# Kernel optimization log

Measured on AMD Instinct MI355X. Metric: run time of the kernel, lower is better.

## Reference

```python
import jax, jax.numpy as jnp
import numpy as np

B, S, D = 4, 1024, 2048
H, KVH, HD = 32, 8, 64
N_REP = H // KVH  # 4
ROPE_THETA = 1000000.0


def _rope_tables(seq_len, head_dim, theta):
    inv_freq = 1.0 / (theta ** (np.arange(0, head_dim, 2, dtype=np.float32) / head_dim))
    t = np.arange(seq_len, dtype=np.float32)
    freqs = np.outer(t, inv_freq)                      # (S, HD/2)
    emb = np.concatenate([freqs, freqs], axis=-1)      # (S, HD)
    return jnp.asarray(np.cos(emb)), jnp.asarray(np.sin(emb))


def setup_inputs() -> dict:
    key = jax.random.key(0)
    kx, kq, kk, kv, ko = jax.random.split(key, 5)
    cos, sin = _rope_tables(S, HD, ROPE_THETA)
    s = 0.02
    return {
        "x": jax.random.normal(kx, (B, S, D), jnp.float32),
        "cos": cos,
        "sin": sin,
        "Wq": jax.random.normal(kq, (D, H * HD), jnp.float32) * s,
        "Wk": jax.random.normal(kk, (D, KVH * HD), jnp.float32) * s,
        "Wv": jax.random.normal(kv, (D, KVH * HD), jnp.float32) * s,
        "Wo": jax.random.normal(ko, (H * HD, D), jnp.float32) * s,
    }


def _rotate_half(t):
    t1, t2 = jnp.split(t, 2, axis=-1)
    return jnp.concatenate([-t2, t1], axis=-1)


def reference(x, cos, sin, Wq, Wk, Wv, Wo):
    # projections
    q = (x @ Wq).reshape(B, S, H, HD)      # (b, s, h, d)
    k = (x @ Wk).reshape(B, S, KVH, HD)
    v = (x @ Wv).reshape(B, S, KVH, HD)

    # RoPE: cos/sin (s, d) broadcast over heads (unsqueeze_dim=1 -> (s,1,d))
    c = cos[:, None, :]
    sn = sin[:, None, :]
    q = q * c + _rotate_half(q) * sn
    k = k * c + _rotate_half(k) * sn

    # GQA attention without physically repeating KV:
    # q grouped as (b, kvh, n_rep, s, d); repeat_kv '(h r)' maps q head g*n_rep+r -> kv head g
    qg = q.transpose(0, 2, 1, 3).reshape(B, KVH, N_REP, S, HD)
    kt = k.transpose(0, 2, 1, 3)  # (b, kvh, s, d)
    vt = v.transpose(0, 2, 1, 3)

    scale = 1.0 / jnp.sqrt(jnp.asarray(HD, x.dtype))
    scores = jnp.einsum('bgrqd,bgkd->bgrqk', qg, kt) * scale  # (b, kvh, rep, s, s)
    probs = jax.nn.softmax(scores, axis=-1)
    out = jnp.einsum('bgrqk,bgkd->bgrqd', probs, vt)           # (b, kvh, rep, s, d)

    out = out.reshape(B, H, S, HD).transpose(0, 2, 1, 3).reshape(B, S, H * HD)
    return out @ Wo
```

## Files before the change

### kernel.cpp

```cpp
#include <hip/hip_runtime.h>

typedef unsigned short u16;
typedef __attribute__((ext_vector_type(8))) __bf16 bf16x8;
typedef __attribute__((ext_vector_type(4))) _Float16 f16x4;
typedef __attribute__((ext_vector_type(8))) _Float16 f16x8;
typedef __attribute__((ext_vector_type(4))) float f32x4;

#define BB 4
#define SS 1024
#define DD 2048
#define HH 32
#define KVHN 8
#define HDIM 64

__device__ __forceinline__ u16 f2b(float f) {
    union { float f; unsigned u; } v; v.f = f;
    unsigned r = v.u + 0x7FFFu + ((v.u >> 16) & 1u);
    return (u16)(r >> 16);
}
__device__ __forceinline__ float b2f(u16 h) {
    union { unsigned u; float f; } v; v.u = ((unsigned)h) << 16; return v.f;
}

__device__ __forceinline__ f32x4 mfma16(bf16x8 a, bf16x8 b, f32x4 c) {
    return __builtin_amdgcn_mfma_f32_16x16x32_bf16(a, b, c, 0, 0, 0);
}
__device__ __forceinline__ f32x4 mfma16h(f16x8 a, f16x8 b, f32x4 c) {
    return __builtin_amdgcn_mfma_f32_16x16x32_f16(a, b, c, 0, 0, 0);
}

__device__ __forceinline__ void async_cp16(const void* g, void* l) {
    __builtin_amdgcn_global_load_lds((__attribute__((address_space(1))) void*)g,
                                     (__attribute__((address_space(3))) void*)l,
                                     16, 0, 0);
}

__device__ __forceinline__ f16x8 pack8_f16(const float* p) {
    union { unsigned u[4]; f16x8 v; } pu;
    pu.u[0] = __builtin_bit_cast(unsigned, __builtin_amdgcn_cvt_pkrtz(p[0], p[1]));
    pu.u[1] = __builtin_bit_cast(unsigned, __builtin_amdgcn_cvt_pkrtz(p[2], p[3]));
    pu.u[2] = __builtin_bit_cast(unsigned, __builtin_amdgcn_cvt_pkrtz(p[4], p[5]));
    pu.u[3] = __builtin_bit_cast(unsigned, __builtin_amdgcn_cvt_pkrtz(p[6], p[7]));
    return pu.v;
}

__global__ __launch_bounds__(256) void cast_x_kernel(const float* __restrict__ x,
                                                     u16* __restrict__ xb) {
    int i = (blockIdx.x * 256 + threadIdx.x) * 4;
    float4 v = *(const float4*)(x + i);
    unsigned r0 = (unsigned)f2b(v.x) | ((unsigned)f2b(v.y) << 16);
    unsigned r1 = (unsigned)f2b(v.z) | ((unsigned)f2b(v.w) << 16);
    *(uint2*)(xb + i) = make_uint2(r0, r1);
}

__global__ __launch_bounds__(256) void wtrans_all_kernel(const float* __restrict__ Wq,
                                                         const float* __restrict__ Wk,
                                                         const float* __restrict__ Wv,
                                                         const float* __restrict__ Wo,
                                                         u16* __restrict__ Wqkvt,
                                                         u16* __restrict__ Wot) {
    __shared__ float tile[32][33];
    int z = blockIdx.z;
    const float* W = (z == 0) ? Wq : (z == 1) ? Wk : (z == 2) ? Wv : Wo;
    int N = (z == 1 || z == 2) ? 512 : 2048;
    int n_off = (z == 1) ? 2048 : (z == 2) ? 2560 : 0;
    u16* Wt = (z == 3) ? Wot : Wqkvt;
    int n0 = blockIdx.x * 32;
    if (n0 >= N) return;
    int k0 = blockIdx.y * 32;
    int tid = threadIdx.x;
    int nj = tid & 31;
    int ki = tid >> 5;
#pragma unroll
    for (int it = 0; it < 4; it++) {
        int kk = it * 8 + ki;
        tile[kk][nj] = W[(size_t)(k0 + kk) * N + n0 + nj];
    }
    __syncthreads();
#pragma unroll
    for (int it = 0; it < 4; it++) {
        int nn = it * 8 + ki;
        Wt[(size_t)(n0 + nn + n_off) * 2048 + k0 + nj] = f2b(tile[nj][nn]);
    }
}

template <int OUT_BF16>
__device__ __forceinline__ void gemm_bt_body(const u16* __restrict__ A,
                                             const u16* __restrict__ Bt,
                                             void* __restrict__ Cv,
                                             int M, int N, int K) {
    __shared__ __align__(16) u16 As[128 * 64];
    __shared__ __align__(16) u16 Bs[128 * 64];
    const int tid = threadIdx.x;
    const int lane = tid & 63;
    const int w = tid >> 6;
    const int m0 = blockIdx.y * 128;
    const int n0 = blockIdx.x * 128;
    const int wm = (w >> 1) * 64;
    const int wn = (w & 1) * 64;
    const int lr = lane & 15;
    const int lg = lane >> 4;
    const int lq = lg * 4;

    const f32x4 zero4 = {0.f, 0.f, 0.f, 0.f};
    f32x4 acc[4][4];
#pragma unroll
    for (int i = 0; i < 4; i++)
#pragma unroll
        for (int j = 0; j < 4; j++) acc[i][j] = zero4;

    for (int k0 = 0; k0 < K; k0 += 64) {
#pragma unroll
        for (int sh = 0; sh < 4; sh++) {
            int i_lin = sh * 256 + tid;
            int row = i_lin >> 3;
            int c = i_lin & 7;
            int cs = c ^ (row & 7);
            async_cp16(A + (size_t)(m0 + row) * K + k0 + cs * 8, As + sh * 2048 + w * 512);
            async_cp16(Bt + (size_t)(n0 + row) * K + k0 + cs * 8, Bs + sh * 2048 + w * 512);
        }
        __syncthreads();
#pragma unroll
        for (int kb = 0; kb < 2; kb++) {
            bf16x8 af[4], bfr[4];
#pragma unroll
            for (int mi = 0; mi < 4; mi++) {
                int r = wm + mi * 16 + lr;
                af[mi] = *(const bf16x8*)(As + r * 64 + (((kb * 4 + lg) ^ (r & 7)) * 8));
            }
#pragma unroll
            for (int ni = 0; ni < 4; ni++) {
                int r = wn + ni * 16 + lr;
                bfr[ni] = *(const bf16x8*)(Bs + r * 64 + (((kb * 4 + lg) ^ (r & 7)) * 8));
            }
#pragma unroll
            for (int mi = 0; mi < 4; mi++)
#pragma unroll
                for (int ni = 0; ni < 4; ni++)
                    acc[mi][ni] = mfma16(af[mi], bfr[ni], acc[mi][ni]);
        }
        __syncthreads();
    }

    if (OUT_BF16) {
        u16* C = (u16*)Cv;
#pragma unroll
        for (int mi = 0; mi < 4; mi++)
#pragma unroll
            for (int ni = 0; ni < 4; ni++)
#pragma unroll
                for (int i = 0; i < 4; i++) {
                    int r = m0 + wm + mi * 16 + lq + i;
                    int c = n0 + wn + ni * 16 + lr;
                    C[(size_t)r * N + c] = f2b(acc[mi][ni][i]);
                }
    } else {
        float* C = (float*)Cv;
#pragma unroll
        for (int mi = 0; mi < 4; mi++)
#pragma unroll
            for (int ni = 0; ni < 4; ni++)
#pragma unroll
                for (int i = 0; i < 4; i++) {
                    int r = m0 + wm + mi * 16 + lq + i;
                    int c = n0 + wn + ni * 16 + lr;
                    C[(size_t)r * N + c] = acc[mi][ni][i];
                }
    }
}

__global__ __launch_bounds__(256) void gemm_qkv(const u16* __restrict__ A,
                                                const u16* __restrict__ Bt,
                                                void* __restrict__ Cv,
                                                int M, int N, int K) {
    gemm_bt_body<1>(A, Bt, Cv, M, N, K);
}

__global__ __launch_bounds__(256) void gemm_out(const u16* __restrict__ A,
                                                const u16* __restrict__ Bt,
                                                void* __restrict__ Cv,
                                                int M, int N, int K) {
    gemm_bt_body<0>(A, Bt, Cv, M, N, K);
}

__global__ __launch_bounds__(256) void rope_kernel(const u16* __restrict__ QKV,
                                                   const float* __restrict__ cosT,
                                                   const float* __restrict__ sinT,
                                                   u16* __restrict__ Qh,
                                                   u16* __restrict__ Kh) {
    const float QSC = 0.125f * 1.44269504088896f;
    int idx = blockIdx.x * 256 + threadIdx.x;
    int d = idx & 31;
    int t = idx >> 5;
    int hh = t % 40;
    int row = t / 40;
    int s = row & (SS - 1);
    int b = row >> 10;
    float c = cosT[s * HDIM + d];
    float sn = sinT[s * HDIM + d];
    if (hh < 32) {
        const u16* src = QKV + (size_t)row * 3072 + hh * 64 + d;
        float x1 = b2f(src[0]), x2 = b2f(src[32]);
        u16* dst = Qh + ((size_t)(b * HH + hh) * SS + s) * 64 + d;
        dst[0] = f2b((x1 * c - x2 * sn) * QSC);
        dst[32] = f2b((x2 * c + x1 * sn) * QSC);
    } else {
        int g = hh - 32;
        const u16* src = QKV + (size_t)row * 3072 + 2048 + g * 64 + d;
        float x1 = b2f(src[0]), x2 = b2f(src[32]);
        int rr = s & 7;
        int kpos = (s & ~31) + ((rr >= 4) ? 16 : 0) + ((s >> 3) & 3) * 4 + (rr & 3);
        u16* dst = Kh + ((size_t)(b * KVHN + g) * SS + kpos) * 64 + d;
        dst[0] = f2b(x1 * c - x2 * sn);
        dst[32] = f2b(x2 * c + x1 * sn);
    }
}

__global__ __launch_bounds__(256) void vtrans_kernel(const u16* __restrict__ QKV,
                                                     u16* __restrict__ Vt) {
    __shared__ u16 tile[64][65];
    int blk = blockIdx.x;
    int st = blk & 15;
    int t2 = blk >> 4;
    int g = t2 & 7;
    int b = t2 >> 3;
    int tid = threadIdx.x;
    int cj = tid & 63;
    int ri = tid >> 6;
    const u16* src = QKV + ((size_t)(b * SS + st * 64)) * 3072 + 2560 + g * 64;
#pragma unroll
    for (int it = 0; it < 16; it++) {
        int s_i = it * 4 + ri;
        tile[s_i][cj] = src[(size_t)s_i * 3072 + cj];
    }
    __syncthreads();
    u16* dst = Vt + ((size_t)(b * KVHN + g) * HDIM) * SS + st * 64;
#pragma unroll
    for (int it = 0; it < 16; it++) {
        int hd_i = it * 4 + ri;
        _Float16 hv = (_Float16)b2f(tile[cj][hd_i]);
        union { _Float16 h; u16 u; } cv; cv.h = hv;
        dst[(size_t)hd_i * SS + cj] = cv.u;
    }
}

__global__ __launch_bounds__(256, 4) void flash_kernel(const u16* __restrict__ Qh,
                                                       const u16* __restrict__ Kh,
                                                       const u16* __restrict__ Vt,
                                                       u16* __restrict__ Attn) {
    __shared__ __align__(16) u16 Kls[2][4096];
    __shared__ __align__(16) u16 Vls[2][4096];
    const int tid = threadIdx.x;
    const int lane = tid & 63;
    const int w = tid >> 6;
    const int qt = blockIdx.x;
    const int g = blockIdx.y;
    const int b = blockIdx.z;
    const int h = g * 4 + w;
    const int lr = lane & 15;
    const int lg = lane >> 4;
    const int lk8 = lg * 8;
    const int lq = lg * 4;

    const u16* Qbase = Qh + ((size_t)(b * HH + h) * SS + qt * 32) * HDIM;
    bf16x8 qb[2][2];
#pragma unroll
    for (int j = 0; j < 2; j++) {
        qb[j][0] = *(const bf16x8*)(Qbase + (size_t)(j * 16 + lr) * HDIM + lk8);
        qb[j][1] = *(const bf16x8*)(Qbase + (size_t)(j * 16 + lr) * HDIM + 32 + lk8);
    }

    const u16* Kbase = Kh + (size_t)(b * KVHN + g) * SS * HDIM;
    const u16* Vbase = Vt + (size_t)(b * KVHN + g) * HDIM * SS;

    const int r0 = tid >> 3;
    const int c0 = tid & 7;

    const f32x4 zero4 = {0.f, 0.f, 0.f, 0.f};
    const f32x4 initS = {-4.f, -4.f, -4.f, -4.f};
    f32x4 o[2][4];
    float lsum[2] = {0.f, 0.f};
#pragma unroll
    for (int j = 0; j < 2; j++)
#pragma unroll
        for (int i = 0; i < 4; i++) o[j][i] = zero4;

#define STAGE(kt, p)                                                              \
    {                                                                             \
        _Pragma("unroll") for (int sh = 0; sh < 2; sh++) {                        \
            int rr = r0 + sh * 32;                                                \
            int cs = c0 ^ (rr & 7);                                               \
            async_cp16(Kbase + (size_t)((kt) + rr) * HDIM + cs * 8,               \
                       &Kls[p][sh * 2048 + w * 512]);                             \
            async_cp16(Vbase + (size_t)rr * SS + (kt) + cs * 8,                   \
                       &Vls[p][sh * 2048 + w * 512]);                             \
        }                                                                         \
    }

    STAGE(0, 0);
    __syncthreads();

    for (int t = 0; t < 16; t++) {
        const int p = t & 1;
        if (t < 15) STAGE((t + 1) * 64, p ^ 1);

#pragma unroll
        for (int c = 0; c < 2; c++) {
            f32x4 s[2][2];
#pragma unroll
            for (int halfi = 0; halfi < 2; halfi++) {
                const int R = c * 32 + halfi * 16 + lr;
                const u16* kr = &Kls[p][R * 64];
                bf16x8 kb0 = *(const bf16x8*)(kr + ((lg ^ (R & 7)) * 8));
                bf16x8 kb1 = *(const bf16x8*)(kr + (((4 + lg) ^ (R & 7)) * 8));
#pragma unroll
                for (int j = 0; j < 2; j++) {
                    f32x4 a = initS;
                    a = mfma16(kb0, qb[j][0], a);
                    a = mfma16(kb1, qb[j][1], a);
                    s[halfi][j] = a;
                }
            }

            f16x8 va[4];
#pragma unroll
            for (int hdt = 0; hdt < 4; hdt++) {
                const int R2 = hdt * 16 + lr;
                va[hdt] = *(const f16x8*)(&Vls[p][R2 * 64 + (((c * 4 + lg) ^ (R2 & 7)) * 8)]);
            }

#pragma unroll
            for (int j = 0; j < 2; j++) {
                float pv[8];
#pragma unroll
                for (int r = 0; r < 4; r++) {
                    pv[r] = __builtin_amdgcn_exp2f(s[0][j][r]);
                    pv[4 + r] = __builtin_amdgcn_exp2f(s[1][j][r]);
                }
                lsum[j] += ((pv[0] + pv[1]) + (pv[2] + pv[3])) +
                           ((pv[4] + pv[5]) + (pv[6] + pv[7]));
                f16x8 pb = pack8_f16(pv);
#pragma unroll
                for (int hdt = 0; hdt < 4; hdt++)
                    o[j][hdt] = mfma16h(va[hdt], pb, o[j][hdt]);
            }
        }
        __syncthreads();
    }

#pragma unroll
    for (int j = 0; j < 2; j++) {
        float su = lsum[j];
        su += __shfl_xor(su, 16);
        su += __shfl_xor(su, 32);
        float inv = 1.f / su;
        u16* Ob = Attn + ((size_t)(b * SS + qt * 32 + j * 16 + lr)) * 2048 + h * 64;
#pragma unroll
        for (int hdt = 0; hdt < 4; hdt++) {
            unsigned r0p = (unsigned)f2b(o[j][hdt][0] * inv) | ((unsigned)f2b(o[j][hdt][1] * inv) << 16);
            unsigned r1p = (unsigned)f2b(o[j][hdt][2] * inv) | ((unsigned)f2b(o[j][hdt][3] * inv) << 16);
            *(uint2*)(Ob + hdt * 16 + lq) = make_uint2(r0p, r1p);
        }
    }
}

extern "C" void kernel_launch(void* const* d_in, const int* in_sizes, int n_in,
                              void* d_out, int out_size, void* d_ws, size_t ws_size,
                              hipStream_t stream) {
    (void)in_sizes; (void)n_in; (void)out_size; (void)ws_size;
    const float* x = (const float*)d_in[0];
    const float* cosT = (const float*)d_in[1];
    const float* sinT = (const float*)d_in[2];
    const float* Wq = (const float*)d_in[3];
    const float* Wk = (const float*)d_in[4];
    const float* Wv = (const float*)d_in[5];
    const float* Wo = (const float*)d_in[6];
    float* out = (float*)d_out;

    char* ws = (char*)d_ws;
    u16* Xb    = (u16*)(ws);
    u16* Wqkvt = (u16*)(ws + 16777216);
    u16* Wot   = (u16*)(ws + 29360128);
    u16* QKV   = (u16*)(ws + 37748736);
    u16* Qh    = (u16*)(ws + 62914560);
    u16* Kh    = (u16*)(ws + 79691776);
    u16* Vt    = (u16*)(ws + 83886080);
    u16* Attn  = (u16*)(ws + 88080384);

    cast_x_kernel<<<8192, 256, 0, stream>>>(x, Xb);
    wtrans_all_kernel<<<dim3(64, 64, 4), 256, 0, stream>>>(Wq, Wk, Wv, Wo, Wqkvt, Wot);

    gemm_qkv<<<dim3(24, 32), 256, 0, stream>>>(Xb, Wqkvt, (void*)QKV, 4096, 3072, 2048);

    rope_kernel<<<20480, 256, 0, stream>>>(QKV, cosT, sinT, Qh, Kh);
    vtrans_kernel<<<512, 256, 0, stream>>>(QKV, Vt);

    flash_kernel<<<dim3(32, 8, 4), 256, 0, stream>>>(Qh, Kh, Vt, Attn);

    gemm_out<<<dim3(16, 32), 256, 0, stream>>>(Attn, Wot, (void*)out, 4096, 2048, 2048);
}
```

Before: 291.4 us.

## Rewrite GEMMs with larger tiles and 4-stage async LDS pipeline

Replaces the shared GEMM body with two specialised kernels that use 512-thread blocks, larger 256x256 / 256x128 tiles, and a 4-buffer global_load_lds ring with K-step 32. The next stages' loads are issued during MFMA work, and a single raw s_barrier per iteration replaces the two __syncthreads. MFMA sections also get s_setprio. This targets load latency exposure and sync overhead in the projection GEMMs. In exchange it uses more LDS per block, fewer blocks (192 and 256), and hard-coded dimensions.

After: 278.1 us. 1.05x faster.

```diff
diff --git a/kernel.cpp b/kernel.cpp
--- a/kernel.cpp
+++ b/kernel.cpp
@@ -33,6 +33,12 @@
     __builtin_amdgcn_global_load_lds((__attribute__((address_space(1))) void*)g,
                                      (__attribute__((address_space(3))) void*)l,
                                      16, 0, 0);
+}
+
+__device__ __forceinline__ void block_sync() {
+    asm volatile("" ::: "memory");
+    __builtin_amdgcn_s_barrier();
+    asm volatile("" ::: "memory");
 }
 
 __device__ __forceinline__ f16x8 pack8_f16(const float* p) {
@@ -84,103 +90,195 @@
     }
 }
 
-template <int OUT_BF16>
-__device__ __forceinline__ void gemm_bt_body(const u16* __restrict__ A,
-                                             const u16* __restrict__ Bt,
-                                             void* __restrict__ Cv,
-                                             int M, int N, int K) {
-    __shared__ __align__(16) u16 As[128 * 64];
-    __shared__ __align__(16) u16 Bs[128 * 64];
+__global__ __launch_bounds__(512, 2) void gemm_qkv(const u16* __restrict__ A,
+                                                   const u16* __restrict__ Bt,
+                                                   u16* __restrict__ C) {
+    __shared__ __align__(16) u16 Ls[4][16384];
     const int tid = threadIdx.x;
     const int lane = tid & 63;
     const int w = tid >> 6;
-    const int m0 = blockIdx.y * 128;
+    const int m0 = blockIdx.y * 256;
+    const int n0 = blockIdx.x * 256;
+    const int wm = (w >> 2) * 128;
+    const int wn = (w & 3) * 64;
+    const int lr = lane & 15;
+    const int lg = lane >> 4;
+
+    const int srow = w * 16 + (lane >> 2);
+    const int sg = (lane & 3) ^ ((srow >> 1) & 3);
+    const u16* ap = A + (size_t)(m0 + srow) * 2048 + sg * 8;
+    const u16* bp = Bt + (size_t)(n0 + srow) * 2048 + sg * 8;
+
+#define QSTAGE_A(pb_, kt_)                                                       \
+    {                                                                            \
+        async_cp16(ap + (kt_) * 32, &Ls[pb_][0] + w * 512);                      \
+        async_cp16(ap + (kt_) * 32 + 128 * 2048, &Ls[pb_][4096] + w * 512);      \
+    }
+#define QSTAGE_B(pb_, kt_)                                                       \
+    {                                                                            \
+        async_cp16(bp + (kt_) * 32, &Ls[pb_][8192] + w * 512);                   \
+        async_cp16(bp + (kt_) * 32 + 128 * 2048, &Ls[pb_][12288] + w * 512);     \
+    }
+
+    f32x4 acc[8][4];
+    const f32x4 zero4 = {0.f, 0.f, 0.f, 0.f};
+#pragma unroll
+    for (int i = 0; i < 8; i++)
+#pragma unroll
+        for (int j = 0; j < 4; j++) acc[i][j] = zero4;
+
+    QSTAGE_A(0, 0); QSTAGE_B(0, 0);
+    QSTAGE_A(1, 1); QSTAGE_B(1, 1);
+    QSTAGE_A(2, 2); QSTAGE_B(2, 2);
+    asm volatile("s_waitcnt vmcnt(8)" ::: "memory");
+    block_sync();
+
+#pragma unroll 4
+    for (int t = 0; t < 64; ++t) {
+        const int bufi = t & 3;
+        const int pb = (t + 3) & 3;
+        const int pt = (t + 3) & 63;
+        const u16* Ab = &Ls[bufi][0];
+        const u16* Bb = &Ls[bufi][8192];
+
+        bf16x8 af[4], bfr[4];
+#pragma unroll
+        for (int ni = 0; ni < 4; ni++) {
+            int r = wn + ni * 16 + lr;
+            bfr[ni] = *(const bf16x8*)(Bb + r * 32 + ((lg ^ ((r >> 1) & 3)) * 8));
+        }
+#pragma unroll
+        for (int mi = 0; mi < 4; mi++) {
+            int r = wm + mi * 16 + lr;
+            af[mi] = *(const bf16x8*)(Ab + r * 32 + ((lg ^ ((r >> 1) & 3)) * 8));
+        }
+        QSTAGE_A(pb, pt);
+        __builtin_amdgcn_s_setprio(1);
+#pragma unroll
+        for (int mi = 0; mi < 4; mi++)
+#pragma unroll
+            for (int ni = 0; ni < 4; ni++)
+                acc[mi][ni] = mfma16(af[mi], bfr[ni], acc[mi][ni]);
+        __builtin_amdgcn_s_setprio(0);
+
+#pragma unroll
+        for (int mi = 0; mi < 4; mi++) {
+            int r = wm + 64 + mi * 16 + lr;
+            af[mi] = *(const bf16x8*)(Ab + r * 32 + ((lg ^ ((r >> 1) & 3)) * 8));
+        }
+        QSTAGE_B(pb, pt);
+        __builtin_amdgcn_s_setprio(1);
+#pragma unroll
+        for (int mi = 0; mi < 4; mi++)
+#pragma unroll
+            for (int ni = 0; ni < 4; ni++)
+                acc[4 + mi][ni] = mfma16(af[mi], bfr[ni], acc[4 + mi][ni]);
+        __builtin_amdgcn_s_setprio(0);
+
+        asm volatile("s_waitcnt vmcnt(8)" ::: "memory");
+        block_sync();
+    }
+    asm volatile("s_waitcnt vmcnt(0)" ::: "memory");
+
+    const int lq = lg * 4;
+#pragma unroll
+    for (int mi = 0; mi < 8; mi++)
+#pragma unroll
+        for (int ni = 0; ni < 4; ni++)
+#pragma unroll
+            for (int i = 0; i < 4; i++) {
+                int r = m0 + wm + mi * 16 + lq + i;
+                int c = n0 + wn + ni * 16 + lr;
+                C[(size_t)r * 3072 + c] = f2b(acc[mi][ni][i]);
+            }
+#undef QSTAGE_A
+#undef QSTAGE_B
+}
+
+__global__ __launch_bounds__(512, 2) void gemm_out(const u16* __restrict__ A,
+                                                   const u16* __restrict__ Bt,
+                                                   float* __restrict__ C) {
+    __shared__ __align__(16) u16 Ls[4][12288];
+    const int tid = threadIdx.x;
+    const int lane = tid & 63;
+    const int w = tid >> 6;
+    const int m0 = blockIdx.y * 256;
     const int n0 = blockIdx.x * 128;
     const int wm = (w >> 1) * 64;
     const int wn = (w & 1) * 64;
     const int lr = lane & 15;
     const int lg = lane >> 4;
+
+    const int srow = w * 16 + (lane >> 2);
+    const int sg = (lane & 3) ^ ((srow >> 1) & 3);
+    const u16* ap = A + (size_t)(m0 + srow) * 2048 + sg * 8;
+    const u16* bp = Bt + (size_t)(n0 + srow) * 2048 + sg * 8;
+
+#define OSTAGE(pb_, kt_)                                                         \
+    {                                                                            \
+        async_cp16(ap + (kt_) * 32, &Ls[pb_][0] + w * 512);                      \
+        async_cp16(ap + (kt_) * 32 + 128 * 2048, &Ls[pb_][4096] + w * 512);      \
+        async_cp16(bp + (kt_) * 32, &Ls[pb_][8192] + w * 512);                   \
+    }
+
+    f32x4 acc[4][4];
+    const f32x4 zero4 = {0.f, 0.f, 0.f, 0.f};
+#pragma unroll
+    for (int i = 0; i < 4; i++)
+#pragma unroll
+        for (int j = 0; j < 4; j++) acc[i][j] = zero4;
+
+    OSTAGE(0, 0);
+    OSTAGE(1, 1);
+    OSTAGE(2, 2);
+    asm volatile("s_waitcnt vmcnt(6)" ::: "memory");
+    block_sync();
+
+#pragma unroll 4
+    for (int t = 0; t < 64; ++t) {
+        const int bufi = t & 3;
+        const int pb = (t + 3) & 3;
+        const int pt = (t + 3) & 63;
+        const u16* Ab = &Ls[bufi][0];
+        const u16* Bb = &Ls[bufi][8192];
+
+        bf16x8 af[4], bfr[4];
+#pragma unroll
+        for (int ni = 0; ni < 4; ni++) {
+            int r = wn + ni * 16 + lr;
+            bfr[ni] = *(const bf16x8*)(Bb + r * 32 + ((lg ^ ((r >> 1) & 3)) * 8));
+        }
+#pragma unroll
+        for (int mi = 0; mi < 4; mi++) {
+            int r = wm + mi * 16 + lr;
+            af[mi] = *(const bf16x8*)(Ab + r * 32 + ((lg ^ ((r >> 1) & 3)) * 8));
+        }
+        OSTAGE(pb, pt);
+        __builtin_amdgcn_s_setprio(1);
+#pragma unroll
+        for (int mi = 0; mi < 4; mi++)
+#pragma unroll
+            for (int ni = 0; ni < 4; ni++)
+                acc[mi][ni] = mfma16(af[mi], bfr[ni], acc[mi][ni]);
+        __builtin_amdgcn_s_setprio(0);
+
+        asm volatile("s_waitcnt vmcnt(6)" ::: "memory");
+        block_sync();
+    }
+    asm volatile("s_waitcnt vmcnt(0)" ::: "memory");
+
     const int lq = lg * 4;
-
-    const f32x4 zero4 = {0.f, 0.f, 0.f, 0.f};
-    f32x4 acc[4][4];
-#pragma unroll
-    for (int i = 0; i < 4; i++)
-#pragma unroll
-        for (int j = 0; j < 4; j++) acc[i][j] = zero4;
-
-    for (int k0 = 0; k0 < K; k0 += 64) {
-#pragma unroll
-        for (int sh = 0; sh < 4; sh++) {
-            int i_lin = sh * 256 + tid;
-            int row = i_lin >> 3;
-            int c = i_lin & 7;
-            int cs = c ^ (row & 7);
-            async_cp16(A + (size_t)(m0 + row) * K + k0 + cs * 8, As + sh * 2048 + w * 512);
-            async_cp16(Bt + (size_t)(n0 + row) * K + k0 + cs * 8, Bs + sh * 2048 + w * 512);
-        }
-        __syncthreads();
-#pragma unroll
-        for (int kb = 0; kb < 2; kb++) {
-            bf16x8 af[4], bfr[4];
-#pragma unroll
-            for (int mi = 0; mi < 4; mi++) {
-                int r = wm + mi * 16 + lr;
-                af[mi] = *(const bf16x8*)(As + r * 64 + (((kb * 4 + lg) ^ (r & 7)) * 8));
+#pragma unroll
+    for (int mi = 0; mi < 4; mi++)
+#pragma unroll
+        for (int ni = 0; ni < 4; ni++)
+#pragma unroll
+            for (int i = 0; i < 4; i++) {
+                int r = m0 + wm + mi * 16 + lq + i;
+                int c = n0 + wn + ni * 16 + lr;
+                C[(size_t)r * 2048 + c] = acc[mi][ni][i];
             }
-#pragma unroll
-            for (int ni = 0; ni < 4; ni++) {
-                int r = wn + ni * 16 + lr;
-                bfr[ni] = *(const bf16x8*)(Bs + r * 64 + (((kb * 4 + lg) ^ (r & 7)) * 8));
-            }
-#pragma unroll
-            for (int mi = 0; mi < 4; mi++)
-#pragma unroll
-                for (int ni = 0; ni < 4; ni++)
-                    acc[mi][ni] = mfma16(af[mi], bfr[ni], acc[mi][ni]);
-        }
-        __syncthreads();
-    }
-
-    if (OUT_BF16) {
-        u16* C = (u16*)Cv;
-#pragma unroll
-        for (int mi = 0; mi < 4; mi++)
-#pragma unroll
-            for (int ni = 0; ni < 4; ni++)
-#pragma unroll
-                for (int i = 0; i < 4; i++) {
-                    int r = m0 + wm + mi * 16 + lq + i;
-                    int c = n0 + wn + ni * 16 + lr;
-                    C[(size_t)r * N + c] = f2b(acc[mi][ni][i]);
-                }
-    } else {
-        float* C = (float*)Cv;
-#pragma unroll
-        for (int mi = 0; mi < 4; mi++)
-#pragma unroll
-            for (int ni = 0; ni < 4; ni++)
-#pragma unroll
-                for (int i = 0; i < 4; i++) {
-                    int r = m0 + wm + mi * 16 + lq + i;
-                    int c = n0 + wn + ni * 16 + lr;
-                    C[(size_t)r * N + c] = acc[mi][ni][i];
-                }
-    }
-}
-
-__global__ __launch_bounds__(256) void gemm_qkv(const u16* __restrict__ A,
-                                                const u16* __restrict__ Bt,
-                                                void* __restrict__ Cv,
-                                                int M, int N, int K) {
-    gemm_bt_body<1>(A, Bt, Cv, M, N, K);
-}
-
-__global__ __launch_bounds__(256) void gemm_out(const u16* __restrict__ A,
-                                                const u16* __restrict__ Bt,
-                                                void* __restrict__ Cv,
-                                                int M, int N, int K) {
-    gemm_bt_body<0>(A, Bt, Cv, M, N, K);
+#undef OSTAGE
 }
 
 __global__ __launch_bounds__(256) void rope_kernel(const u16* __restrict__ QKV,
@@ -390,12 +488,12 @@
     cast_x_kernel<<<8192, 256, 0, stream>>>(x, Xb);
     wtrans_all_kernel<<<dim3(64, 64, 4), 256, 0, stream>>>(Wq, Wk, Wv, Wo, Wqkvt, Wot);
 
-    gemm_qkv<<<dim3(24, 32), 256, 0, stream>>>(Xb, Wqkvt, (void*)QKV, 4096, 3072, 2048);
+    gemm_qkv<<<dim3(12, 16), 512, 0, stream>>>(Xb, Wqkvt, QKV);
 
     rope_kernel<<<20480, 256, 0, stream>>>(QKV, cosT, sinT, Qh, Kh);
     vtrans_kernel<<<512, 256, 0, stream>>>(QKV, Vt);
 
     flash_kernel<<<dim3(32, 8, 4), 256, 0, stream>>>(Qh, Kh, Vt, Attn);
 
-    gemm_out<<<dim3(16, 32), 256, 0, stream>>>(Attn, Wot, (void*)out, 4096, 2048, 2048);
-}
+    gemm_out<<<dim3(16, 16), 512, 0, stream>>>(Attn, Wot, out);
+}
```

## Rewrite projection GEMMs with 256-wide tiles, fine-grained pipelining, XCD-aware block mapping

Applied to the files above, without the earlier changes.

Replaces the generic 128x128 GEMM with specialized 512-thread kernels that use 256x256 (QKV) and 256x128 (output) tiles. They double-buffer K-halves in LDS with interleaved async loads and raw barriers, and raise wave priority around MFMA bursts. Block indices are remapped so that tiles sharing A/B rows land on the same XCD for L2 reuse, and the flash kernel grid is flattened with a similar XCD-aware remap. This aims to cut LDS/global traffic per FLOP and improve cache locality. The cost is higher register pressure and a hardcoded-shape, hand-tuned schedule that depends on exact vmcnt accounting.

Measured after the change: 270.5 us. -7.2%, faster.

```diff
diff --git a/kernel.cpp b/kernel.cpp
--- a/kernel.cpp
+++ b/kernel.cpp
@@ -33,6 +33,12 @@
     __builtin_amdgcn_global_load_lds((__attribute__((address_space(1))) void*)g,
                                      (__attribute__((address_space(3))) void*)l,
                                      16, 0, 0);
+}
+
+__device__ __forceinline__ void block_sync() {
+    asm volatile("" ::: "memory");
+    __builtin_amdgcn_s_barrier();
+    asm volatile("" ::: "memory");
 }
 
 __device__ __forceinline__ f16x8 pack8_f16(const float* p) {
@@ -84,103 +90,242 @@
     }
 }
 
-template <int OUT_BF16>
-__device__ __forceinline__ void gemm_bt_body(const u16* __restrict__ A,
-                                             const u16* __restrict__ Bt,
-                                             void* __restrict__ Cv,
-                                             int M, int N, int K) {
-    __shared__ __align__(16) u16 As[128 * 64];
-    __shared__ __align__(16) u16 Bs[128 * 64];
+__global__ __launch_bounds__(512, 2) void gemm_qkv(const u16* __restrict__ A,
+                                                   const u16* __restrict__ Bt,
+                                                   u16* __restrict__ C) {
+    __shared__ __align__(16) u16 Ls[2][32768];
     const int tid = threadIdx.x;
     const int lane = tid & 63;
     const int w = tid >> 6;
-    const int m0 = blockIdx.y * 128;
-    const int n0 = blockIdx.x * 128;
-    const int wm = (w >> 1) * 64;
-    const int wn = (w & 1) * 64;
+
+    const int bid = blockIdx.x;
+    const int xcd = bid & 7;
+    const int loc = bid >> 3;
+    const int mt = (xcd & 3) * 4 + (loc & 3);
+    const int nt = (xcd >> 2) * 6 + (loc >> 2);
+    const int m0 = mt * 256;
+    const int n0 = nt * 256;
+
+    const int wm = (w >> 2) * 128;
+    const int wn = (w & 3) * 64;
     const int lr = lane & 15;
     const int lg = lane >> 4;
+
+    const int row0 = tid >> 2;
+    const int g = tid & 3;
+    const int sg = g ^ ((row0 >> 1) & 3);
+    const u16* pA0 = A + (size_t)(m0 + row0) * 2048 + sg * 8;
+    const u16* pA1 = pA0 + (size_t)128 * 2048;
+    const u16* pB0 = Bt + (size_t)(n0 + row0) * 2048 + sg * 8;
+    const u16* pB1 = pB0 + (size_t)128 * 2048;
+
+#define QSTA(buf_, ks_, T_)                                                     \
+    {                                                                           \
+        async_cp16(pA0 + (T_) * 64 + (ks_) * 32, &Ls[buf_][(ks_) * 8192 + w * 512]);        \
+        async_cp16(pA1 + (T_) * 64 + (ks_) * 32, &Ls[buf_][(ks_) * 8192 + 4096 + w * 512]); \
+    }
+#define QSTB(buf_, ks_, T_)                                                     \
+    {                                                                           \
+        async_cp16(pB0 + (T_) * 64 + (ks_) * 32, &Ls[buf_][16384 + (ks_) * 8192 + w * 512]);        \
+        async_cp16(pB1 + (T_) * 64 + (ks_) * 32, &Ls[buf_][16384 + (ks_) * 8192 + 4096 + w * 512]); \
+    }
+
+    f32x4 acc[8][4];
+    const f32x4 zero4 = {0.f, 0.f, 0.f, 0.f};
+#pragma unroll
+    for (int i = 0; i < 8; i++)
+#pragma unroll
+        for (int j = 0; j < 4; j++) acc[i][j] = zero4;
+
+    bf16x8 af[8], bfr[4];
+
+#define QLDA(ks_)                                                               \
+    _Pragma("unroll") for (int mi = 0; mi < 8; mi++) {                          \
+        int r_ = wm + mi * 16 + lr;                                             \
+        af[mi] = *(const bf16x8*)(&Ls[cur][(ks_) * 8192 + r_ * 32 + ((lg ^ ((r_ >> 1) & 3)) * 8)]); \
+    }
+#define QLDB(ks_, nb_)                                                          \
+    _Pragma("unroll") for (int q_ = 0; q_ < 2; q_++) {                          \
+        int ni_ = (nb_) * 2 + q_;                                               \
+        int r_ = wn + ni_ * 16 + lr;                                            \
+        bfr[ni_] = *(const bf16x8*)(&Ls[cur][16384 + (ks_) * 8192 + r_ * 32 + ((lg ^ ((r_ >> 1) & 3)) * 8)]); \
+    }
+#define QMM(nb_)                                                                \
+    __builtin_amdgcn_s_setprio(1);                                              \
+    _Pragma("unroll") for (int mi = 0; mi < 8; mi++) _Pragma("unroll") for (int q_ = 0; q_ < 2; q_++) { \
+        int ni_ = (nb_) * 2 + q_;                                               \
+        acc[mi][ni_] = mfma16(af[mi], bfr[ni_], acc[mi][ni_]);                  \
+    }                                                                           \
+    __builtin_amdgcn_s_setprio(0);
+#define QWAITMM                                                                 \
+    asm volatile("s_waitcnt lgkmcnt(0)" ::: "memory");                          \
+    __builtin_amdgcn_sched_barrier(0);
+
+    QSTA(0, 0, 0); QSTB(0, 0, 0); QSTA(0, 1, 0); QSTB(0, 1, 0);
+    QSTA(1, 0, 1); QSTB(1, 0, 1);
+    asm volatile("s_waitcnt vmcnt(4)" ::: "memory");
+    block_sync();
+
+#pragma unroll 2
+    for (int T = 0; T < 32; ++T) {
+        const int cur = T & 1;
+        const int oth = cur ^ 1;
+        const int Tp1 = (T + 1) & 31;
+        const int Tp2 = (T + 2) & 31;
+
+        QLDA(0); QLDB(0, 0);
+        QSTA(oth, 1, Tp1);
+        block_sync(); QWAITMM;
+        QMM(0);
+        block_sync();
+        QLDB(0, 1);
+        QSTB(oth, 1, Tp1);
+        block_sync(); QWAITMM;
+        QMM(1);
+        block_sync();
+        QLDA(1); QLDB(1, 0);
+        QSTA(cur, 0, Tp2);
+        block_sync(); QWAITMM;
+        QMM(0);
+        block_sync();
+        QLDB(1, 1);
+        QSTB(cur, 0, Tp2);
+        block_sync(); QWAITMM;
+        QMM(1);
+        asm volatile("s_waitcnt vmcnt(4)" ::: "memory");
+        block_sync();
+    }
+    asm volatile("s_waitcnt vmcnt(0)" ::: "memory");
+
     const int lq = lg * 4;
-
+#pragma unroll
+    for (int mi = 0; mi < 8; mi++)
+#pragma unroll
+        for (int ni = 0; ni < 4; ni++)
+#pragma unroll
+            for (int i = 0; i < 4; i++) {
+                int r = m0 + wm + mi * 16 + lq + i;
+                int c = n0 + wn + ni * 16 + lr;
+                C[(size_t)r * 3072 + c] = f2b(acc[mi][ni][i]);
+            }
+#undef QSTA
+#undef QSTB
+#undef QLDA
+#undef QLDB
+#undef QMM
+#undef QWAITMM
+}
+
+__global__ __launch_bounds__(512, 2) void gemm_out(const u16* __restrict__ A,
+                                                   const u16* __restrict__ Bt,
+                                                   float* __restrict__ C) {
+    __shared__ __align__(16) u16 Ls[2][24576];
+    const int tid = threadIdx.x;
+    const int lane = tid & 63;
+    const int w = tid >> 6;
+
+    const int bid = blockIdx.x;
+    const int xcd = bid & 7;
+    const int loc = bid >> 3;
+    const int mt = (xcd & 3) * 4 + (loc & 3);
+    const int nt = (xcd >> 2) * 8 + (loc >> 2);
+    const int m0 = mt * 256;
+    const int n0 = nt * 128;
+
+    const int wm = (w >> 2) * 128;
+    const int wn = (w & 3) * 32;
+    const int lr = lane & 15;
+    const int lg = lane >> 4;
+
+    const int row0 = tid >> 2;
+    const int g = tid & 3;
+    const int sg = g ^ ((row0 >> 1) & 3);
+    const u16* pA0 = A + (size_t)(m0 + row0) * 2048 + sg * 8;
+    const u16* pA1 = pA0 + (size_t)128 * 2048;
+    const u16* pB0 = Bt + (size_t)(n0 + row0) * 2048 + sg * 8;
+
+#define OSTA(buf_, ks_, T_)                                                     \
+    {                                                                           \
+        async_cp16(pA0 + (T_) * 64 + (ks_) * 32, &Ls[buf_][(ks_) * 8192 + w * 512]);        \
+        async_cp16(pA1 + (T_) * 64 + (ks_) * 32, &Ls[buf_][(ks_) * 8192 + 4096 + w * 512]); \
+    }
+#define OSTB(buf_, ks_, T_)                                                     \
+    {                                                                           \
+        async_cp16(pB0 + (T_) * 64 + (ks_) * 32, &Ls[buf_][16384 + (ks_) * 4096 + w * 512]); \
+    }
+
+    f32x4 acc[8][2];
     const f32x4 zero4 = {0.f, 0.f, 0.f, 0.f};
-    f32x4 acc[4][4];
-#pragma unroll
-    for (int i = 0; i < 4; i++)
-#pragma unroll
-        for (int j = 0; j < 4; j++) acc[i][j] = zero4;
-
-    for (int k0 = 0; k0 < K; k0 += 64) {
-#pragma unroll
-        for (int sh = 0; sh < 4; sh++) {
-            int i_lin = sh * 256 + tid;
-            int row = i_lin >> 3;
-            int c = i_lin & 7;
-            int cs = c ^ (row & 7);
-            async_cp16(A + (size_t)(m0 + row) * K + k0 + cs * 8, As + sh * 2048 + w * 512);
-            async_cp16(Bt + (size_t)(n0 + row) * K + k0 + cs * 8, Bs + sh * 2048 + w * 512);
-        }
-        __syncthreads();
-#pragma unroll
-        for (int kb = 0; kb < 2; kb++) {
-            bf16x8 af[4], bfr[4];
-#pragma unroll
-            for (int mi = 0; mi < 4; mi++) {
-                int r = wm + mi * 16 + lr;
-                af[mi] = *(const bf16x8*)(As + r * 64 + (((kb * 4 + lg) ^ (r & 7)) * 8));
+#pragma unroll
+    for (int i = 0; i < 8; i++)
+#pragma unroll
+        for (int j = 0; j < 2; j++) acc[i][j] = zero4;
+
+    bf16x8 af[8], bfr[2];
+
+#define OLDA(ks_)                                                               \
+    _Pragma("unroll") for (int mi = 0; mi < 8; mi++) {                          \
+        int r_ = wm + mi * 16 + lr;                                             \
+        af[mi] = *(const bf16x8*)(&Ls[cur][(ks_) * 8192 + r_ * 32 + ((lg ^ ((r_ >> 1) & 3)) * 8)]); \
+    }
+#define OLDB(ks_)                                                               \
+    _Pragma("unroll") for (int ni = 0; ni < 2; ni++) {                          \
+        int r_ = wn + ni * 16 + lr;                                             \
+        bfr[ni] = *(const bf16x8*)(&Ls[cur][16384 + (ks_) * 4096 + r_ * 32 + ((lg ^ ((r_ >> 1) & 3)) * 8)]); \
+    }
+#define OMM                                                                     \
+    __builtin_amdgcn_s_setprio(1);                                              \
+    _Pragma("unroll") for (int mi = 0; mi < 8; mi++) _Pragma("unroll") for (int ni = 0; ni < 2; ni++) { \
+        acc[mi][ni] = mfma16(af[mi], bfr[ni], acc[mi][ni]);                     \
+    }                                                                           \
+    __builtin_amdgcn_s_setprio(0);
+#define OWAITMM                                                                 \
+    asm volatile("s_waitcnt lgkmcnt(0)" ::: "memory");                          \
+    __builtin_amdgcn_sched_barrier(0);
+
+    OSTA(0, 0, 0); OSTB(0, 0, 0); OSTA(0, 1, 0); OSTB(0, 1, 0);
+    OSTA(1, 0, 1); OSTB(1, 0, 1);
+    asm volatile("s_waitcnt vmcnt(3)" ::: "memory");
+    block_sync();
+
+#pragma unroll 2
+    for (int T = 0; T < 32; ++T) {
+        const int cur = T & 1;
+        const int oth = cur ^ 1;
+        const int Tp1 = (T + 1) & 31;
+        const int Tp2 = (T + 2) & 31;
+
+        OLDA(0); OLDB(0);
+        OSTA(oth, 1, Tp1); OSTB(oth, 1, Tp1);
+        block_sync(); OWAITMM;
+        OMM;
+        block_sync();
+        OLDA(1); OLDB(1);
+        OSTA(cur, 0, Tp2); OSTB(cur, 0, Tp2);
+        block_sync(); OWAITMM;
+        OMM;
+        asm volatile("s_waitcnt vmcnt(3)" ::: "memory");
+        block_sync();
+    }
+    asm volatile("s_waitcnt vmcnt(0)" ::: "memory");
+
+    const int lq = lg * 4;
+#pragma unroll
+    for (int mi = 0; mi < 8; mi++)
+#pragma unroll
+        for (int ni = 0; ni < 2; ni++)
+#pragma unroll
+            for (int i = 0; i < 4; i++) {
+                int r = m0 + wm + mi * 16 + lq + i;
+                int c = n0 + wn + ni * 16 + lr;
+                C[(size_t)r * 2048 + c] = acc[mi][ni][i];
             }
-#pragma unroll
-            for (int ni = 0; ni < 4; ni++) {
-                int r = wn + ni * 16 + lr;
-                bfr[ni] = *(const bf16x8*)(Bs + r * 64 + (((kb * 4 + lg) ^ (r & 7)) * 8));
-            }
-#pragma unroll
-            for (int mi = 0; mi < 4; mi++)
-#pragma unroll
-                for (int ni = 0; ni < 4; ni++)
-                    acc[mi][ni] = mfma16(af[mi], bfr[ni], acc[mi][ni]);
-        }
-        __syncthreads();
-    }
-
-    if (OUT_BF16) {
-        u16* C = (u16*)Cv;
-#pragma unroll
-        for (int mi = 0; mi < 4; mi++)
-#pragma unroll
-            for (int ni = 0; ni < 4; ni++)
-#pragma unroll
-                for (int i = 0; i < 4; i++) {
-                    int r = m0 + wm + mi * 16 + lq + i;
-                    int c = n0 + wn + ni * 16 + lr;
-                    C[(size_t)r * N + c] = f2b(acc[mi][ni][i]);
-                }
-    } else {
-        float* C = (float*)Cv;
-#pragma unroll
-        for (int mi = 0; mi < 4; mi++)
-#pragma unroll
-            for (int ni = 0; ni < 4; ni++)
-#pragma unroll
-                for (int i = 0; i < 4; i++) {
-                    int r = m0 + wm + mi * 16 + lq + i;
-                    int c = n0 + wn + ni * 16 + lr;
-                    C[(size_t)r * N + c] = acc[mi][ni][i];
-                }
-    }
-}
-
-__global__ __launch_bounds__(256) void gemm_qkv(const u16* __restrict__ A,
-                                                const u16* __restrict__ Bt,
-                                                void* __restrict__ Cv,
-                                                int M, int N, int K) {
-    gemm_bt_body<1>(A, Bt, Cv, M, N, K);
-}
-
-__global__ __launch_bounds__(256) void gemm_out(const u16* __restrict__ A,
-                                                const u16* __restrict__ Bt,
-                                                void* __restrict__ Cv,
-                                                int M, int N, int K) {
-    gemm_bt_body<0>(A, Bt, Cv, M, N, K);
+#undef OSTA
+#undef OSTB
+#undef OLDA
+#undef OLDB
+#undef OMM
+#undef OWAITMM
 }
 
 __global__ __launch_bounds__(256) void rope_kernel(const u16* __restrict__ QKV,
@@ -253,9 +398,11 @@
     const int tid = threadIdx.x;
     const int lane = tid & 63;
     const int w = tid >> 6;
-    const int qt = blockIdx.x;
-    const int g = blockIdx.y;
-    const int b = blockIdx.z;
+    const int bid = blockIdx.x;
+    const int gbp = ((bid & 7) << 2) | ((bid >> 3) & 3);
+    const int qt = bid >> 5;
+    const int g = gbp & 7;
+    const int b = gbp >> 3;
     const int h = g * 4 + w;
     const int lr = lane & 15;
     const int lg = lane >> 4;
@@ -289,7 +436,7 @@
     {                                                                             \
         _Pragma("unroll") for (int sh = 0; sh < 2; sh++) {                        \
             int rr = r0 + sh * 32;                                                \
-            int cs = c0 ^ (rr & 7);                                               \
+            int cs = c0 ^ (rr & 7);                                              \
             async_cp16(Kbase + (size_t)((kt) + rr) * HDIM + cs * 8,               \
                        &Kls[p][sh * 2048 + w * 512]);                             \
             async_cp16(Vbase + (size_t)rr * SS + (kt) + cs * 8,                   \
@@ -390,12 +537,12 @@
     cast_x_kernel<<<8192, 256, 0, stream>>>(x, Xb);
     wtrans_all_kernel<<<dim3(64, 64, 4), 256, 0, stream>>>(Wq, Wk, Wv, Wo, Wqkvt, Wot);
 
-    gemm_qkv<<<dim3(24, 32), 256, 0, stream>>>(Xb, Wqkvt, (void*)QKV, 4096, 3072, 2048);
+    gemm_qkv<<<192, 512, 0, stream>>>(Xb, Wqkvt, QKV);
 
     rope_kernel<<<20480, 256, 0, stream>>>(QKV, cosT, sinT, Qh, Kh);
     vtrans_kernel<<<512, 256, 0, stream>>>(QKV, Vt);
 
-    flash_kernel<<<dim3(32, 8, 4), 256, 0, stream>>>(Qh, Kh, Vt, Attn);
-
-    gemm_out<<<dim3(16, 32), 256, 0, stream>>>(Attn, Wot, (void*)out, 4096, 2048, 2048);
-}
+    flash_kernel<<<1024, 256, 0, stream>>>(Qh, Kh, Vt, Attn);
+
+    gemm_out<<<256, 512, 0, stream>>>(Attn, Wot, out);
+}
```
